# Performance work log

Hardware: AMD Instinct MI355X
Metric: run time of the kernel (lower is better)

Reference implementation:

```python
import jax, jax.numpy as jnp
import numpy as np

B = 262144
D = 16
G = 20000


def setup_inputs() -> dict:
    key = jax.random.key(0)
    ks = jax.random.split(key, 20)
    lin = lambda k, o, i: jax.random.normal(k, (o, i), jnp.float32) * (1.0 / np.sqrt(i))
    inp = {
        "x": jax.random.randint(ks[0], (B, 2), 0, G),
        "phenos": jax.random.normal(ks[1], (B, 2), jnp.float32),
        "emb": jax.random.normal(ks[2], (G, D), jnp.float32),
        "W1": lin(ks[3], D, D), "b1": jnp.zeros((D,), jnp.float32),
        "W2": lin(ks[4], D, D), "b2": jnp.zeros((D,), jnp.float32),
        "W3": lin(ks[5], D, D), "b3": jnp.zeros((D,), jnp.float32),
        # bilinear weights: small noise + stacked identity, as in the torch init
        "BW": 0.01 * jax.random.normal(ks[6], (D, D, D), jnp.float32)
              + jnp.broadcast_to(jnp.eye(D, dtype=jnp.float32)[None, :, :], (D, D, D)),
        "BD": 0.01 * jax.random.normal(ks[7], (D, D), jnp.float32) + 1.0,
        "Boff": 0.01 * jax.random.normal(ks[8], (D,), jnp.float32),
        "Wc1": lin(ks[9], D, D), "bc1": jnp.zeros((D,), jnp.float32),
        "Wc2": lin(ks[10], 1, D), "bc2": jnp.zeros((1,), jnp.float32),
    }
    return inp


def reference(x, phenos, emb, W1, b1, W2, b2, W3, b3, BW, BD, Boff, Wc1, bc1, Wc2, bc2):
    # embedding lookup: [B, 2, D] -> flatten gene axis into batch
    h = emb[x].reshape(-1, D)
    # embedding_ffn (dropout is identity in eval): Linear->ReLU->Linear->ReLU->Linear
    h = jax.nn.relu(h @ W1.T + b1)
    h = jax.nn.relu(h @ W2.T + b2)
    h = (h @ W3.T + b3).reshape(-1, 2, D)
    e0, e1 = h[:, 0, :], h[:, 1, :]  # [B, D] each
    # torch: x0 = BW.matmul(e0.T).T  -> x0[b,m,n] = sum_k BW[n,m,k] e0[b,k]
    A = jnp.einsum("nmk,bk->bmn", BW, e0)  # [B, D, D]
    # torch: x1 = BW.matmul(e1.T).T, *= BD, permute -> C[b,m,n] = sum_k BW[m,n,k] e1[b,k], scaled by BD[n,m]
    C = jnp.einsum("mnk,bk->bmn", BW, e1)  # [B, D, D]
    z = jnp.einsum("bmn,bmn,nm->bn", A, C, BD) + Boff  # [B, D]
    # embedding_comb: Linear->ReLU->Linear(D,1)
    z = jax.nn.relu(z @ Wc1.T + bc1)
    z = z @ Wc2.T + bc2  # [B, 1]
    return jnp.sum(phenos, axis=1) + z[:, 0]
```

## Files before the change

kernel.cpp:

```cpp
#include <hip/hip_runtime.h>
#include <hip/hip_bf16.h>

#define D  16
#define NB 262144
#define NG 20000
#define ROWPITCH 36
#define ZPITCH   20

typedef __attribute__((ext_vector_type(8))) short bf16x8;
typedef __attribute__((ext_vector_type(4))) float f32x4;
typedef __attribute__((ext_vector_type(2))) float f32x2;

__device__ __forceinline__ unsigned pack_hi16(unsigned b0, unsigned b1) {
    return __builtin_amdgcn_perm(b1, b0, 0x07060302u);
}

__global__ void __launch_bounds__(256)
prep_kernel(const float* __restrict__ emb,
            const float* __restrict__ W1, const float* __restrict__ b1,
            const float* __restrict__ W2, const float* __restrict__ b2,
            const float* __restrict__ W3, const float* __restrict__ b3,
            const float* __restrict__ BW, const float* __restrict__ BD,
            const float* __restrict__ Wc1, const float* __restrict__ bc1,
            const float* __restrict__ Boff,
            float* __restrict__ T, short* __restrict__ Bhi, short* __restrict__ Blo,
            float* __restrict__ bc1p) {
    __shared__ float smem[8704];
    int tid = threadIdx.x;
    int blk = blockIdx.x;

    if (blk < 79) {
        int g = blk * 256 + tid;
        if (g >= NG) return;
        float h[D], t[D];
        const float4* ep = (const float4*)(emb + (size_t)g * D);
        float4 v0 = ep[0], v1 = ep[1], v2 = ep[2], v3 = ep[3];
        h[0]=v0.x; h[1]=v0.y; h[2]=v0.z; h[3]=v0.w;
        h[4]=v1.x; h[5]=v1.y; h[6]=v1.z; h[7]=v1.w;
        h[8]=v2.x; h[9]=v2.y; h[10]=v2.z; h[11]=v2.w;
        h[12]=v3.x; h[13]=v3.y; h[14]=v3.z; h[15]=v3.w;
        #pragma unroll
        for (int i = 0; i < D; ++i) {
            float a = b1[i];
            #pragma unroll
            for (int d = 0; d < D; ++d) a = fmaf(W1[i * D + d], h[d], a);
            t[i] = fmaxf(a, 0.f);
        }
        #pragma unroll
        for (int i = 0; i < D; ++i) {
            float a = b2[i];
            #pragma unroll
            for (int d = 0; d < D; ++d) a = fmaf(W2[i * D + d], t[d], a);
            h[i] = fmaxf(a, 0.f);
        }
        #pragma unroll
        for (int i = 0; i < D; ++i) {
            float a = b3[i];
            #pragma unroll
            for (int d = 0; d < D; ++d) a = fmaf(W3[i * D + d], h[d], a);
            t[i] = a;
        }
        float4* tp = (float4*)(T + (size_t)g * D);
        tp[0] = make_float4(t[0], t[1], t[2], t[3]);
        tp[1] = make_float4(t[4], t[5], t[6], t[7]);
        tp[2] = make_float4(t[8], t[9], t[10], t[11]);
        tp[3] = make_float4(t[12], t[13], t[14], t[15]);
        return;
    }

    float* bwS = smem;
    float* bdS = smem + 4096;
    float* MmS = smem + 4352;
    #pragma unroll
    for (int i = 0; i < 16; ++i) bwS[tid + 256 * i] = BW[tid + 256 * i];
    bdS[tid] = BD[tid];
    __syncthreads();

    int n = tid >> 4, j = tid & 15;
    float acc[16];
    #pragma unroll
    for (int k = 0; k < 16; ++k) acc[k] = 0.f;
    #pragma unroll
    for (int m = 0; m < 16; ++m) {
        float sw = bdS[n * 16 + m] * bwS[(m * 16 + n) * 16 + j];
        const f32x4* w1 = (const f32x4*)&bwS[(n * 16 + m) * 16];
        #pragma unroll
        for (int q = 0; q < 4; ++q) {
            f32x4 w = w1[q];
            acc[4 * q + 0] = fmaf(sw, w.x, acc[4 * q + 0]);
            acc[4 * q + 1] = fmaf(sw, w.y, acc[4 * q + 1]);
            acc[4 * q + 2] = fmaf(sw, w.z, acc[4 * q + 2]);
            acc[4 * q + 3] = fmaf(sw, w.w, acc[4 * q + 3]);
        }
    }
    #pragma unroll
    for (int k = 0; k < 16; ++k) MmS[(k * 16 + j) * 17 + n] = acc[k];
    __syncthreads();

    for (int idx = tid; idx < 512; idx += 256) {
        int s = idx >> 6, lane = idx & 63;
        int q = lane >> 4, nn = lane & 15;
        unsigned hw[4], lw[4];
        #pragma unroll
        for (int w = 0; w < 4; ++w) {
            int kk0 = s * 32 + q * 8 + 2 * w;
            float v0 = MmS[kk0 * 17 + nn], v1 = MmS[(kk0 + 1) * 17 + nn];
            unsigned b0 = __float_as_uint(v0), b1 = __float_as_uint(v1);
            float h0 = __uint_as_float(b0 & 0xFFFF0000u);
            float h1 = __uint_as_float(b1 & 0xFFFF0000u);
            hw[w] = pack_hi16(b0, b1);
            lw[w] = pack_hi16(__float_as_uint(v0 - h0), __float_as_uint(v1 - h1));
        }
        ((uint4*)Bhi)[idx] = make_uint4(hw[0], hw[1], hw[2], hw[3]);
        ((uint4*)Blo)[idx] = make_uint4(lw[0], lw[1], lw[2], lw[3]);
    }

    if (tid < 16) {
        float a = bc1[tid];
        #pragma unroll
        for (int nn = 0; nn < 16; ++nn) a += Wc1[tid * 16 + nn] * Boff[nn];
        bc1p[tid] = a;
    }
}

__global__ void __launch_bounds__(256)
main_kernel(const int* __restrict__ x, const float* __restrict__ phenos,
            const float* __restrict__ T,
            const short* __restrict__ Bhi, const short* __restrict__ Blo,
            const float* __restrict__ bc1p, const float* __restrict__ Wc1,
            const float* __restrict__ Wc2, const float* __restrict__ bc2,
            float* __restrict__ out) {
    __shared__ float smem[9216];
    int tid  = threadIdx.x;
    int wave = tid >> 6, lane = tid & 63;
    int quad = lane >> 4, nl = lane & 15;
    long base = (long)blockIdx.x * 256 + wave * 64;
    float* stg = smem + wave * 2304;

    bf16x8 bh[8], bl[8];
    #pragma unroll
    for (int s = 0; s < 8; ++s) {
        bh[s] = ((const bf16x8*)Bhi)[s * 64 + lane];
        bl[s] = ((const bf16x8*)Blo)[s * 64 + lane];
    }

    long r = base + lane;
    int2 g = ((const int2*)x)[r];
    {
        const f32x4* p0 = (const f32x4*)(T + g.x * 16);
        const f32x4* p1 = (const f32x4*)(T + g.y * 16);
        f32x4 c0 = p0[0], c1 = p0[1], c2 = p0[2], c3 = p0[3];
        f32x4 c4 = p1[0], c5 = p1[1], c6 = p1[2], c7 = p1[3];
        f32x4* wp = (f32x4*)(stg + lane * ROWPITCH);
        wp[0] = c0; wp[1] = c1; wp[2] = c2; wp[3] = c3;
        wp[4] = c4; wp[5] = c5; wp[6] = c6; wp[7] = c7;
    }
    __syncthreads();

    f32x4 acc[4];
    #pragma unroll
    for (int t = 0; t < 4; ++t) acc[t] = (f32x4){0.f, 0.f, 0.f, 0.f};
    const int par = quad >> 1;
    const int eo  = (quad & 1) * 8;

    #pragma unroll
    for (int t = 0; t < 4; ++t) {
        const float* rowp = stg + (t * 16 + nl) * ROWPITCH;
        float ev[8];
        #pragma unroll
        for (int s = 0; s < 8; ++s) ev[s] = rowp[2 * s + par];
        f32x4 e1a = *(const f32x4*)(rowp + 16 + eo);
        f32x4 e1b = *(const f32x4*)(rowp + 20 + eo);
        float2 e1p[4] = {make_float2(e1a.x, e1a.y), make_float2(e1a.z, e1a.w),
                         make_float2(e1b.x, e1b.y), make_float2(e1b.z, e1b.w)};

        #pragma unroll
        for (int s = 0; s < 8; ++s) {
            unsigned aw[4];
            #pragma unroll
            for (int w = 0; w < 4; ++w) {
                float2 p = make_float2(ev[s] * e1p[w].x, ev[s] * e1p[w].y);
                __hip_bfloat162 hv = __float22bfloat162_rn(p);
                aw[w] = *(unsigned*)&hv;
            }
            bf16x8 ah = __builtin_bit_cast(bf16x8, make_uint4(aw[0], aw[1], aw[2], aw[3]));
            acc[t] = __builtin_amdgcn_mfma_f32_16x16x32_bf16(ah, bh[s], acc[t], 0, 0, 0);
            acc[t] = __builtin_amdgcn_mfma_f32_16x16x32_bf16(ah, bl[s], acc[t], 0, 0, 0);
        }
    }

    __syncthreads();
    float* zb = smem + wave * 1280;
    #pragma unroll
    for (int t = 0; t < 4; ++t) {
        #pragma unroll
        for (int reg = 0; reg < 4; ++reg)
            zb[(t * 16 + quad * 4 + reg) * ZPITCH + nl] = acc[t][reg];
    }
    __syncthreads();

    const float* zr = zb + lane * ZPITCH;
    f32x4 q0 = *(const f32x4*)(zr + 0);
    f32x4 q1 = *(const f32x4*)(zr + 4);
    f32x4 q2 = *(const f32x4*)(zr + 8);
    f32x4 q3 = *(const f32x4*)(zr + 12);
    f32x2 zv2[8] = {(f32x2){q0.x, q0.y}, (f32x2){q0.z, q0.w},
                    (f32x2){q1.x, q1.y}, (f32x2){q1.z, q1.w},
                    (f32x2){q2.x, q2.y}, (f32x2){q2.z, q2.w},
                    (f32x2){q3.x, q3.y}, (f32x2){q3.z, q3.w}};

    const f32x2* w2 = (const f32x2*)Wc1;
    float a2 = bc2[0];
    #pragma unroll
    for (int i = 0; i < 16; ++i) {
        f32x2 u2 = (f32x2){0.f, 0.f};
        #pragma unroll
        for (int n2 = 0; n2 < 8; ++n2) u2 += w2[i * 8 + n2] * zv2[n2];
        float u = u2.x + u2.y + bc1p[i];
        u = fmaxf(u, 0.f);
        a2 = fmaf(Wc2[i], u, a2);
    }

    float2 ph = ((const float2*)phenos)[r];
    out[r] = ph.x + ph.y + a2;
}

extern "C" void kernel_launch(void* const* d_in, const int* in_sizes, int n_in,
                              void* d_out, int out_size, void* d_ws, size_t ws_size,
                              hipStream_t stream) {
    const int*   x      = (const int*)  d_in[0];
    const float* phenos = (const float*)d_in[1];
    const float* emb    = (const float*)d_in[2];
    const float* W1     = (const float*)d_in[3];
    const float* b1     = (const float*)d_in[4];
    const float* W2     = (const float*)d_in[5];
    const float* b2     = (const float*)d_in[6];
    const float* W3     = (const float*)d_in[7];
    const float* b3     = (const float*)d_in[8];
    const float* BW     = (const float*)d_in[9];
    const float* BD     = (const float*)d_in[10];
    const float* Boff   = (const float*)d_in[11];
    const float* Wc1    = (const float*)d_in[12];
    const float* bc1    = (const float*)d_in[13];
    const float* Wc2    = (const float*)d_in[14];
    const float* bc2    = (const float*)d_in[15];
    float* out = (float*)d_out;

    char* wsb = (char*)d_ws;
    short* Bhi  = (short*)(wsb);
    short* Blo  = (short*)(wsb + 8192);
    float* bc1p = (float*)(wsb + 16384);
    float* T    = (float*)(wsb + 16448);

    prep_kernel<<<80, 256, 0, stream>>>(emb, W1, b1, W2, b2, W3, b3, BW, BD,
                                        Wc1, bc1, Boff, T, Bhi, Blo, bc1p);
    main_kernel<<<NB / 256, 256, 0, stream>>>(x, phenos, T, Bhi, Blo, bc1p, Wc1, Wc2, bc2, out);
}
```

Before: 107.9 us.

## Switch bilinear MFMA to single fp16 pass and gather rows via direct-to-LDS loads

After: 104.1 us. -3.6%, faster.

```diff
diff --git a/kernel.cpp b/kernel.cpp
--- a/kernel.cpp
+++ b/kernel.cpp
@@ -4,15 +4,16 @@
 #define D  16
 #define NB 262144
 #define NG 20000
-#define ROWPITCH 36
-#define ZPITCH   20
-
-typedef __attribute__((ext_vector_type(8))) short bf16x8;
+#define ZPITCH 20
+
+typedef __attribute__((ext_vector_type(8))) _Float16 f16x8;
 typedef __attribute__((ext_vector_type(4))) float f32x4;
 typedef __attribute__((ext_vector_type(2))) float f32x2;
 
-__device__ __forceinline__ unsigned pack_hi16(unsigned b0, unsigned b1) {
-    return __builtin_amdgcn_perm(b1, b0, 0x07060302u);
+__device__ __forceinline__ unsigned pack_f16rn(float a, float b) {
+    unsigned short ua = __builtin_bit_cast(unsigned short, (_Float16)a);
+    unsigned short ub = __builtin_bit_cast(unsigned short, (_Float16)b);
+    return (unsigned)ua | ((unsigned)ub << 16);
 }
 
 __global__ void __launch_bounds__(256)
@@ -23,7 +24,7 @@
             const float* __restrict__ BW, const float* __restrict__ BD,
             const float* __restrict__ Wc1, const float* __restrict__ bc1,
             const float* __restrict__ Boff,
-            float* __restrict__ T, short* __restrict__ Bhi, short* __restrict__ Blo,
+            float* __restrict__ T, short* __restrict__ Bh,
             float* __restrict__ bc1p) {
     __shared__ float smem[8704];
     int tid = threadIdx.x;
@@ -100,19 +101,14 @@
     for (int idx = tid; idx < 512; idx += 256) {
         int s = idx >> 6, lane = idx & 63;
         int q = lane >> 4, nn = lane & 15;
-        unsigned hw[4], lw[4];
+        unsigned hw[4];
         #pragma unroll
         for (int w = 0; w < 4; ++w) {
             int kk0 = s * 32 + q * 8 + 2 * w;
             float v0 = MmS[kk0 * 17 + nn], v1 = MmS[(kk0 + 1) * 17 + nn];
-            unsigned b0 = __float_as_uint(v0), b1 = __float_as_uint(v1);
-            float h0 = __uint_as_float(b0 & 0xFFFF0000u);
-            float h1 = __uint_as_float(b1 & 0xFFFF0000u);
-            hw[w] = pack_hi16(b0, b1);
-            lw[w] = pack_hi16(__float_as_uint(v0 - h0), __float_as_uint(v1 - h1));
-        }
-        ((uint4*)Bhi)[idx] = make_uint4(hw[0], hw[1], hw[2], hw[3]);
-        ((uint4*)Blo)[idx] = make_uint4(lw[0], lw[1], lw[2], lw[3]);
+            hw[w] = pack_f16rn(v0, v1);
+        }
+        ((uint4*)Bh)[idx] = make_uint4(hw[0], hw[1], hw[2], hw[3]);
     }
 
     if (tid < 16) {
@@ -126,51 +122,60 @@
 __global__ void __launch_bounds__(256)
 main_kernel(const int* __restrict__ x, const float* __restrict__ phenos,
             const float* __restrict__ T,
-            const short* __restrict__ Bhi, const short* __restrict__ Blo,
+            const short* __restrict__ Bh,
             const float* __restrict__ bc1p, const float* __restrict__ Wc1,
             const float* __restrict__ Wc2, const float* __restrict__ bc2,
             float* __restrict__ out) {
-    __shared__ float smem[9216];
+    __shared__ float smem[8192];
     int tid  = threadIdx.x;
     int wave = tid >> 6, lane = tid & 63;
     int quad = lane >> 4, nl = lane & 15;
     long base = (long)blockIdx.x * 256 + wave * 64;
-    float* stg = smem + wave * 2304;
-
-    bf16x8 bh[8], bl[8];
-    #pragma unroll
-    for (int s = 0; s < 8; ++s) {
-        bh[s] = ((const bf16x8*)Bhi)[s * 64 + lane];
-        bl[s] = ((const bf16x8*)Blo)[s * 64 + lane];
-    }
-
-    long r = base + lane;
-    int2 g = ((const int2*)x)[r];
-    {
-        const f32x4* p0 = (const f32x4*)(T + g.x * 16);
-        const f32x4* p1 = (const f32x4*)(T + g.y * 16);
-        f32x4 c0 = p0[0], c1 = p0[1], c2 = p0[2], c3 = p0[3];
-        f32x4 c4 = p1[0], c5 = p1[1], c6 = p1[2], c7 = p1[3];
-        f32x4* wp = (f32x4*)(stg + lane * ROWPITCH);
-        wp[0] = c0; wp[1] = c1; wp[2] = c2; wp[3] = c3;
-        wp[4] = c4; wp[5] = c5; wp[6] = c6; wp[7] = c7;
-    }
-    __syncthreads();
+    float* stg = smem + wave * 2048;
+
+    f16x8 bh[8];
+    #pragma unroll
+    for (int s = 0; s < 8; ++s) bh[s] = ((const f16x8*)Bh)[s * 64 + lane];
+
+    const int h   = lane >> 3;
+    const int sq  = (lane & 7) ^ h;
+    const int qtr = sq & 3;
+    const int* xw = x + 2 * base;
+    const int goff = 2 * h + (sq >> 2);
+    int gid[8];
+    #pragma unroll
+    for (int i = 0; i < 8; ++i) gid[i] = xw[i * 16 + goff];
+    #pragma unroll
+    for (int i = 0; i < 8; ++i) {
+        const float* src = T + (size_t)(unsigned)gid[i] * 16 + qtr * 4;
+        __builtin_amdgcn_global_load_lds(
+            (const __attribute__((address_space(1))) unsigned*)src,
+            (__attribute__((address_space(3))) unsigned*)(stg + i * 256),
+            16, 0, 0);
+    }
+    asm volatile("s_waitcnt vmcnt(0)" ::: "memory");
+
+    float2 ph = ((const float2*)phenos)[base + lane];
 
     f32x4 acc[4];
     #pragma unroll
     for (int t = 0; t < 4; ++t) acc[t] = (f32x4){0.f, 0.f, 0.f, 0.f};
     const int par = quad >> 1;
-    const int eo  = (quad & 1) * 8;
+    const int b1q = quad & 1;
+    const int nl7 = nl & 7;
 
     #pragma unroll
     for (int t = 0; t < 4; ++t) {
-        const float* rowp = stg + (t * 16 + nl) * ROWPITCH;
+        const float* rowp = stg + (t * 16 + nl) * 32;
         float ev[8];
         #pragma unroll
-        for (int s = 0; s < 8; ++s) ev[s] = rowp[2 * s + par];
-        f32x4 e1a = *(const f32x4*)(rowp + 16 + eo);
-        f32x4 e1b = *(const f32x4*)(rowp + 20 + eo);
+        for (int sp = 0; sp < 4; ++sp) {
+            const float* qp = rowp + ((sp ^ nl7) << 2) + par;
+            ev[2 * sp]     = qp[0];
+            ev[2 * sp + 1] = qp[2];
+        }
+        f32x4 e1a = *(const f32x4*)(rowp + (((4 + 2 * b1q) ^ nl7) << 2));
+        f32x4 e1b = *(const f32x4*)(rowp + (((5 + 2 * b1q) ^ nl7) << 2));
         float2 e1p[4] = {make_float2(e1a.x, e1a.y), make_float2(e1a.z, e1a.w),
                          make_float2(e1b.x, e1b.y), make_float2(e1b.z, e1b.w)};
 
@@ -179,13 +184,12 @@
             unsigned aw[4];
             #pragma unroll
             for (int w = 0; w < 4; ++w) {
-                float2 p = make_float2(ev[s] * e1p[w].x, ev[s] * e1p[w].y);
-                __hip_bfloat162 hv = __float22bfloat162_rn(p);
-                aw[w] = *(unsigned*)&hv;
+                f32x2 p = (f32x2){ev[s] * e1p[w].x, ev[s] * e1p[w].y};
+                auto cv = __builtin_amdgcn_cvt_pkrtz(p.x, p.y);
+                aw[w] = __builtin_bit_cast(unsigned, cv);
             }
-            bf16x8 ah = __builtin_bit_cast(bf16x8, make_uint4(aw[0], aw[1], aw[2], aw[3]));
-            acc[t] = __builtin_amdgcn_mfma_f32_16x16x32_bf16(ah, bh[s], acc[t], 0, 0, 0);
-            acc[t] = __builtin_amdgcn_mfma_f32_16x16x32_bf16(ah, bl[s], acc[t], 0, 0, 0);
+            f16x8 ah = __builtin_bit_cast(f16x8, make_uint4(aw[0], aw[1], aw[2], aw[3]));
+            acc[t] = __builtin_amdgcn_mfma_f32_16x16x32_f16(ah, bh[s], acc[t], 0, 0, 0);
         }
     }
 
@@ -197,7 +201,7 @@
         for (int reg = 0; reg < 4; ++reg)
             zb[(t * 16 + quad * 4 + reg) * ZPITCH + nl] = acc[t][reg];
     }
-    __syncthreads();
+    __builtin_amdgcn_wave_barrier();
 
     const float* zr = zb + lane * ZPITCH;
     f32x4 q0 = *(const f32x4*)(zr + 0);
@@ -221,8 +225,7 @@
         a2 = fmaf(Wc2[i], u, a2);
     }
 
-    float2 ph = ((const float2*)phenos)[r];
-    out[r] = ph.x + ph.y + a2;
+    out[base + lane] = ph.x + ph.y + a2;
 }
 
 extern "C" void kernel_launch(void* const* d_in, const int* in_sizes, int n_in,
@@ -247,12 +250,11 @@
     float* out = (float*)d_out;
 
     char* wsb = (char*)d_ws;
-    short* Bhi  = (short*)(wsb);
-    short* Blo  = (short*)(wsb + 8192);
+    short* Bh   = (short*)(wsb);
     float* bc1p = (float*)(wsb + 16384);
     float* T    = (float*)(wsb + 16448);
 
     prep_kernel<<<80, 256, 0, stream>>>(emb, W1, b1, W2, b2, W3, b3, BW, BD,
-                                        Wc1, bc1, Boff, T, Bhi, Blo, bc1p);
-    main_kernel<<<NB / 256, 256, 0, stream>>>(x, phenos, T, Bhi, Blo, bc1p, Wc1, Wc2, bc2, out);
-}
+                                        Wc1, bc1, Boff, T, Bh, bc1p);
+    main_kernel<<<NB / 256, 256, 0, stream>>>(x, phenos, T, Bh, bc1p, Wc1, Wc2, bc2, out);
+}
```
